# Kernel optimization log

Measured on AMD Instinct MI355X. Metric: run time of the kernel, lower is better.

Reference implementation:

```python
import jax, jax.numpy as jnp
import numpy as np

N_HITS = 49152
HIT_F = 256
INST_F = 32
N_IT_CONST = 1024
Q_MIN = 0.5   # ObjCondensationLoss default q_min
S_B = 1.0     # ObjCondensationLoss default background strength


def setup_inputs() -> dict:
    key = jax.random.key(0)
    ks = jax.random.split(key, 6)
    x = jax.random.normal(ks[0], (N_HITS, HIT_F), jnp.float32)
    W_beta = jax.random.normal(ks[1], (HIT_F, 1), jnp.float32) / np.sqrt(HIT_F).astype(np.float32)
    b_beta = jnp.zeros((1,), jnp.float32)
    W_coord = jax.random.normal(ks[2], (HIT_F, INST_F), jnp.float32) / np.sqrt(HIT_F).astype(np.float32)
    b_coord = jnp.zeros((INST_F,), jnp.float32)
    temp = jnp.zeros((), jnp.float32)  # nn.Parameter(torch.tensor(0.0))
    # true instance labels per hit; pin first N_IT hits so every instance is populated
    y_i = jax.random.randint(ks[3], (N_HITS,), 0, N_IT_CONST)
    y_i = y_i.at[:N_IT_CONST].set(jnp.arange(N_IT_CONST))
    idx = jnp.arange(N_HITS)
    noise = (idx % 5 == 0) & (idx >= N_IT_CONST)
    y_i = jnp.where(noise, -1, y_i).astype(jnp.int64)
    y_semantic = jax.random.randint(ks[4], (N_HITS,), 0, 7).astype(jnp.int32)
    # hit -> true-instance membership edges (E_H_IT), fixed shape built eagerly
    yv = np.asarray(y_i)
    e0 = np.nonzero(yv >= 0)[0]
    edge_index = jnp.asarray(np.stack([e0, yv[e0]]), dtype=jnp.int32)
    return {"x": x, "W_beta": W_beta, "b_beta": b_beta, "W_coord": W_coord,
            "b_coord": b_coord, "temp": temp, "y_i": y_i,
            "y_semantic": y_semantic, "edge_index": edge_index, "n_it": N_IT_CONST}


def _obj_condensation_loss(ox, beta, y_i, edge_index, n_it):
    """Object condensation loss -> stack([background_loss, potential_loss])."""
    n = ox.shape[0]
    beta_c = jnp.clip(beta, 1e-4, 1.0 - 1e-4)
    q = jnp.arctanh(beta_c) ** 2 + Q_MIN  # charge per hit, [N]
    e_h, e_i = edge_index[0], edge_index[1]
    qe = q[e_h]
    # condensation point alpha_k = member hit with max charge (segment argmax)
    seg_max = jax.ops.segment_max(qe, e_i, num_segments=n_it)
    is_max = qe >= seg_max[e_i]
    alpha = jax.ops.segment_min(jnp.where(is_max, e_h, n), e_i, num_segments=n_it)
    alpha = jnp.clip(alpha, 0, n - 1)
    x_a = ox[alpha]        # [K, D]
    q_a = q[alpha]         # [K]
    beta_a = beta_c[alpha]  # [K]
    # attractive potential over membership edges: q_i * q_alpha * ||x_i - x_alpha||^2
    d2_att = jnp.sum((ox[e_h] - x_a[e_i]) ** 2, axis=-1)
    v_att = jnp.sum(qe * q_a[e_i] * d2_att)
    # repulsive potential over all (hit, instance) non-member pairs: hinge(1 - dist)
    d2 = (jnp.sum(ox * ox, axis=1)[:, None] + jnp.sum(x_a * x_a, axis=1)[None, :]
          - 2.0 * ox @ x_a.T)  # [N, K]
    dist = jnp.sqrt(jnp.maximum(d2, 0.0) + 1e-12)
    hinge = jnp.maximum(1.0 - dist, 0.0)
    member = jnp.zeros((n, n_it), jnp.float32).at[e_h, e_i].set(1.0)
    v_rep = jnp.sum((q[:, None] * q_a[None, :]) * hinge * (1.0 - member))
    l_v = (v_att + v_rep) / n
    # background loss: push beta_alpha -> 1, noise-hit beta -> 0
    noise = y_i < 0
    n_noise = jnp.maximum(jnp.sum(noise), 1)
    l_b = jnp.mean(1.0 - beta_a) + S_B * jnp.sum(jnp.where(noise, beta_c, 0.0)) / n_noise
    return jnp.stack([l_b, l_v])


def reference(x, W_beta, b_beta, W_coord, b_coord, temp, y_i, y_semantic, edge_index, n_it):
    beta = jax.nn.sigmoid(x @ W_beta + b_beta)[:, 0]  # h.of, [N]
    ox = x @ W_coord + b_coord                        # h.ox, [N, D]
    loss_vec = _obj_condensation_loss(ox, beta, y_i, edge_index, n_it)
    loss_vec = loss_vec * jnp.exp(-temp)  # temperature-weighted (b, v)
    return loss_vec.sum() + temp          # train-stage scalar loss
```

## Files before the change

kernel.cpp:

```cpp
#include <hip/hip_runtime.h>
#include <math.h>

#define NH 49152
#define KI 1024
#define DD 32
#define HF 256

#define WS_PART   0
#define WS_SEGMAX 8
#define WS_ALPHA  (WS_SEGMAX + KI)
#define WS_XA     (WS_ALPHA + KI)
#define WS_A12    (WS_XA + KI*DD)
#define WS_H12    (WS_A12 + KI*12)
#define WS_OX     (WS_H12 + NH*12)

__global__ void k_init(float* __restrict__ ws) {
    int i = blockIdx.x * blockDim.x + threadIdx.x;
    if (i < KI) {
        ws[WS_SEGMAX + i] = 0.0f;
        ((int*)ws)[WS_ALPHA + i] = NH;
    }
    if (i < 8) ws[WS_PART + i] = 0.0f;
}

__global__ __launch_bounds__(256, 2) void k_gemm(
        const float* __restrict__ x, const float* __restrict__ Wb,
        const float* __restrict__ bb, const float* __restrict__ Wc,
        const float* __restrict__ bcrd, const int* __restrict__ yi,
        float* __restrict__ ws) {
    __shared__ float wl[256 * 36];
    __shared__ float xs[64 * 65];
    const int t  = threadIdx.x;
    const int hl = t & 63;
    const int g  = t >> 6;
    const int h0 = blockIdx.x * 64;

    #pragma unroll
    for (int c4 = 0; c4 < 8; ++c4)
        *(float4*)(wl + t * 36 + c4 * 4) = *(const float4*)(Wc + t * 32 + c4 * 4);
    wl[t * 36 + 32] = Wb[t];

    const int srow = t >> 4;
    const int scol = (t & 15) * 4;
    float4 r0, r1, r2, r3;
#define LOADC(kc) { \
        const float* xp = x + (size_t)(h0 + srow) * HF + (kc) * 64 + scol; \
        r0 = *(const float4*)(xp); \
        r1 = *(const float4*)(xp + 16 * HF); \
        r2 = *(const float4*)(xp + 32 * HF); \
        r3 = *(const float4*)(xp + 48 * HF); }
#define STOREC() { \
        float* d0p = xs + srow * 65 + scol; \
        d0p[0]=r0.x; d0p[1]=r0.y; d0p[2]=r0.z; d0p[3]=r0.w; \
        float* d1p = xs + (srow+16) * 65 + scol; \
        d1p[0]=r1.x; d1p[1]=r1.y; d1p[2]=r1.z; d1p[3]=r1.w; \
        float* d2p = xs + (srow+32) * 65 + scol; \
        d2p[0]=r2.x; d2p[1]=r2.y; d2p[2]=r2.z; d2p[3]=r2.w; \
        float* d3p = xs + (srow+48) * 65 + scol; \
        d3p[0]=r3.x; d3p[1]=r3.y; d3p[2]=r3.z; d3p[3]=r3.w; }

    float acc0 = 0.f, acc1 = 0.f, acc2 = 0.f, acc3 = 0.f;
    float acc4 = 0.f, acc5 = 0.f, acc6 = 0.f, acc7 = 0.f, acc8 = 0.f;

    LOADC(0);
    __syncthreads();
    STOREC();
    __syncthreads();

    for (int kc = 0; kc < 4; ++kc) {
        if (kc < 3) LOADC(kc + 1);
        const float* wbase = wl + kc * 64 * 36 + g * 8;
        #pragma unroll 8
        for (int kk = 0; kk < 64; ++kk) {
            float a = xs[hl * 65 + kk];
            const float4 w0 = *(const float4*)(wbase + kk * 36);
            const float4 w1 = *(const float4*)(wbase + kk * 36 + 4);
            acc0 = fmaf(a, w0.x, acc0);
            acc1 = fmaf(a, w0.y, acc1);
            acc2 = fmaf(a, w0.z, acc2);
            acc3 = fmaf(a, w0.w, acc3);
            acc4 = fmaf(a, w1.x, acc4);
            acc5 = fmaf(a, w1.y, acc5);
            acc6 = fmaf(a, w1.z, acc6);
            acc7 = fmaf(a, w1.w, acc7);
            if (g == 3) acc8 = fmaf(a, wbase[kk * 36 + 8], acc8);
        }
        __syncthreads();
        if (kc < 3) { STOREC(); __syncthreads(); }
    }

    const int h = h0 + hl;
    float4 o0, o1;
    o0.x = acc0 + bcrd[g * 8 + 0];
    o0.y = acc1 + bcrd[g * 8 + 1];
    o0.z = acc2 + bcrd[g * 8 + 2];
    o0.w = acc3 + bcrd[g * 8 + 3];
    o1.x = acc4 + bcrd[g * 8 + 4];
    o1.y = acc5 + bcrd[g * 8 + 5];
    o1.z = acc6 + bcrd[g * 8 + 6];
    o1.w = acc7 + bcrd[g * 8 + 7];
    *(float4*)(ws + WS_OX + (size_t)h * DD + g * 8)     = o0;
    *(float4*)(ws + WS_OX + (size_t)h * DD + g * 8 + 4) = o1;

    if (g == 0) {
        float s8 = o0.x*o0.x + o0.y*o0.y + o0.z*o0.z + o0.w*o0.w
                 + o1.x*o1.x + o1.y*o1.y + o1.z*o1.z + o1.w*o1.w;
        *(float4*)(ws + WS_H12 + (size_t)h * 12)     = o0;
        *(float4*)(ws + WS_H12 + (size_t)h * 12 + 4) = o1;
        ws[WS_H12 + (size_t)h * 12 + 8] = 0.5f * s8;
    }
    if (g == 3) {
        float z    = acc8 + bb[0];
        float beta = 1.0f / (1.0f + expf(-z));
        float bcv  = fminf(fmaxf(beta, 1e-4f), 0.9999f);
        float at   = atanhf(bcv);
        ws[WS_H12 + (size_t)h * 12 + 9]  = at * at + 0.5f;
        ws[WS_H12 + (size_t)h * 12 + 10] = bcv;
        int y = yi[h];
        float    nb  = (y < 0) ? bcv : 0.0f;
        unsigned cnt = (y < 0) ? 1u : 0u;
        for (int off = 32; off > 0; off >>= 1) {
            nb  += __shfl_down(nb, off);
            cnt += __shfl_down(cnt, off);
        }
        if (hl == 0) {
            atomicAdd(ws + WS_PART + 2, nb);
            atomicAdd((unsigned int*)(ws + WS_PART + 3), cnt);
        }
    }
}

__global__ __launch_bounds__(256) void k_segmax(const int* __restrict__ eh, const int* __restrict__ ei,
                                                int E, float* __restrict__ ws) {
    int e = blockIdx.x * 256 + threadIdx.x;
    if (e < E) {
        float qe = ws[WS_H12 + (size_t)eh[e] * 12 + 9];
        atomicMax((unsigned int*)(ws + WS_SEGMAX + ei[e]), __float_as_uint(qe));
    }
}

__global__ __launch_bounds__(256) void k_argmin(const int* __restrict__ eh, const int* __restrict__ ei,
                                                int E, float* __restrict__ ws) {
    int e = blockIdx.x * 256 + threadIdx.x;
    if (e < E) {
        float qe = ws[WS_H12 + (size_t)eh[e] * 12 + 9];
        if (qe >= ws[WS_SEGMAX + ei[e]])
            atomicMin((int*)ws + WS_ALPHA + ei[e], eh[e]);
    }
}

__global__ __launch_bounds__(1024) void k_gather(float* __restrict__ ws) {
    const int k = threadIdx.x;
    int a = ((int*)ws)[WS_ALPHA + k];
    a = min(a, NH - 1);
    float4 v0, v1;
    float s8 = 0.0f;
    #pragma unroll
    for (int d0 = 0; d0 < DD; d0 += 4) {
        float4 v = *(const float4*)(ws + WS_OX + (size_t)a * DD + d0);
        *(float4*)(ws + WS_XA + (size_t)k * DD + d0) = v;
        if (d0 == 0) { v0 = v; s8 += v.x*v.x + v.y*v.y + v.z*v.z + v.w*v.w; }
        if (d0 == 4) { v1 = v; s8 += v.x*v.x + v.y*v.y + v.z*v.z + v.w*v.w; }
    }
    *(float4*)(ws + WS_A12 + (size_t)k * 12)     = v0;
    *(float4*)(ws + WS_A12 + (size_t)k * 12 + 4) = v1;
    ws[WS_A12 + (size_t)k * 12 + 8] = 0.5f * (s8 - 1.0f);
    ws[WS_A12 + (size_t)k * 12 + 9] = ws[WS_H12 + (size_t)a * 12 + 9];
    float omba = 1.0f - ws[WS_H12 + (size_t)a * 12 + 10];
    for (int off = 32; off > 0; off >>= 1) omba += __shfl_down(omba, off);
    __shared__ float red[16];
    if ((k & 63) == 0) red[k >> 6] = omba;
    __syncthreads();
    if (k == 0) {
        float s = 0.0f;
        for (int i = 0; i < 16; ++i) s += red[i];
        atomicAdd(ws + WS_PART + 4, s);
    }
}

__global__ __launch_bounds__(256) void k_att(const int* __restrict__ eh, const int* __restrict__ ei,
                                             int E, float* __restrict__ ws) {
    const int t = threadIdx.x;
    const int e = blockIdx.x * 256 + t;
    float c = 0.0f;
    if (e < E) {
        const int h = eh[e], k = ei[e];
        const float* a = ws + WS_OX + (size_t)h * DD;
        const float* b = ws + WS_XA + (size_t)k * DD;
        float d2 = 0.0f;
        #pragma unroll
        for (int d0 = 0; d0 < DD; d0 += 4) {
            float4 av = *(const float4*)(a + d0);
            float4 bv = *(const float4*)(b + d0);
            float dx = av.x - bv.x; d2 = fmaf(dx, dx, d2);
            float dy = av.y - bv.y; d2 = fmaf(dy, dy, d2);
            float dz = av.z - bv.z; d2 = fmaf(dz, dz, d2);
            float dw = av.w - bv.w; d2 = fmaf(dw, dw, d2);
        }
        c = ws[WS_H12 + (size_t)h * 12 + 9] * ws[WS_A12 + (size_t)k * 12 + 9] * d2;
    }
    for (int off = 32; off > 0; off >>= 1) c += __shfl_down(c, off);
    __shared__ float red[4];
    if ((t & 63) == 0) red[t >> 6] = c;
    __syncthreads();
    if (t == 0) atomicAdd(ws + WS_PART + 1, red[0] + red[1] + red[2] + red[3]);
}

__global__ __launch_bounds__(256, 4) void k_rep(const int* __restrict__ yi, float* __restrict__ ws) {
    __shared__ float al[64 * 12];
    const int t  = threadIdx.x;
    const int bh = blockIdx.x % 96;
    const int bk = blockIdx.x / 96;

    for (int i = t; i < 64 * 12; i += 256)
        al[i] = ws[WS_A12 + (size_t)bk * 64 * 12 + i];
    __syncthreads();

    const int h1 = bh * 512 + t;
    const int h2 = h1 + 256;
    const float4 p0  = *(const float4*)(ws + WS_H12 + (size_t)h1 * 12);
    const float4 p1  = *(const float4*)(ws + WS_H12 + (size_t)h1 * 12 + 4);
    const float2 cq1 = *(const float2*)(ws + WS_H12 + (size_t)h1 * 12 + 8);
    const float4 s0  = *(const float4*)(ws + WS_H12 + (size_t)h2 * 12);
    const float4 s1  = *(const float4*)(ws + WS_H12 + (size_t)h2 * 12 + 4);
    const float2 cq2 = *(const float2*)(ws + WS_H12 + (size_t)h2 * 12 + 8);
    const int yh1 = yi[h1], yh2 = yi[h2];
    float loc = 0.0f;

    #pragma unroll 4
    for (int r = 0; r < 64; ++r) {
        const float4 b0  = *(const float4*)(al + r * 12);
        const float4 b1  = *(const float4*)(al + r * 12 + 4);
        const float2 bcq = *(const float2*)(al + r * 12 + 8);
        float acc1 = -cq1.x - bcq.x;
        acc1 = fmaf(p0.x, b0.x, acc1);
        acc1 = fmaf(p0.y, b0.y, acc1);
        acc1 = fmaf(p0.z, b0.z, acc1);
        acc1 = fmaf(p0.w, b0.w, acc1);
        acc1 = fmaf(p1.x, b1.x, acc1);
        acc1 = fmaf(p1.y, b1.y, acc1);
        acc1 = fmaf(p1.z, b1.z, acc1);
        acc1 = fmaf(p1.w, b1.w, acc1);
        float acc2 = -cq2.x - bcq.x;
        acc2 = fmaf(s0.x, b0.x, acc2);
        acc2 = fmaf(s0.y, b0.y, acc2);
        acc2 = fmaf(s0.z, b0.z, acc2);
        acc2 = fmaf(s0.w, b0.w, acc2);
        acc2 = fmaf(s1.x, b1.x, acc2);
        acc2 = fmaf(s1.y, b1.y, acc2);
        acc2 = fmaf(s1.z, b1.z, acc2);
        acc2 = fmaf(s1.w, b1.w, acc2);
        if (acc1 > 0.0f) {
            const int kg = bk * 64 + r;
            if (yh1 != kg) {
                float d2 = 1.0f - 2.0f * acc1;
                const float* hp = ws + WS_OX + (size_t)h1 * DD;
                const float* ap = ws + WS_XA + (size_t)kg * DD;
                #pragma unroll
                for (int d = 8; d < DD; d += 4) {
                    float4 av = *(const float4*)(hp + d);
                    float4 bv = *(const float4*)(ap + d);
                    float dx = av.x - bv.x; d2 = fmaf(dx, dx, d2);
                    float dy = av.y - bv.y; d2 = fmaf(dy, dy, d2);
                    float dz = av.z - bv.z; d2 = fmaf(dz, dz, d2);
                    float dw = av.w - bv.w; d2 = fmaf(dw, dw, d2);
                }
                float dist = sqrtf(fmaxf(d2, 0.0f) + 1e-12f);
                float hin  = 1.0f - dist;
                if (hin > 0.0f) loc += cq1.y * bcq.y * hin;
            }
        }
        if (acc2 > 0.0f) {
            const int kg = bk * 64 + r;
            if (yh2 != kg) {
                float d2 = 1.0f - 2.0f * acc2;
                const float* hp = ws + WS_OX + (size_t)h2 * DD;
                const float* ap = ws + WS_XA + (size_t)kg * DD;
                #pragma unroll
                for (int d = 8; d < DD; d += 4) {
                    float4 av = *(const float4*)(hp + d);
                    float4 bv = *(const float4*)(ap + d);
                    float dx = av.x - bv.x; d2 = fmaf(dx, dx, d2);
                    float dy = av.y - bv.y; d2 = fmaf(dy, dy, d2);
                    float dz = av.z - bv.z; d2 = fmaf(dz, dz, d2);
                    float dw = av.w - bv.w; d2 = fmaf(dw, dw, d2);
                }
                float dist = sqrtf(fmaxf(d2, 0.0f) + 1e-12f);
                float hin  = 1.0f - dist;
                if (hin > 0.0f) loc += cq2.y * bcq.y * hin;
            }
        }
    }
    for (int off = 32; off > 0; off >>= 1) loc += __shfl_down(loc, off);
    __shared__ float red[4];
    if ((t & 63) == 0) red[t >> 6] = loc;
    __syncthreads();
    if (t == 0) atomicAdd(ws + WS_PART + 0, red[0] + red[1] + red[2] + red[3]);
}

__global__ void k_final(const float* __restrict__ temp, float* __restrict__ ws,
                        float* __restrict__ out) {
    float vrep  = ws[WS_PART + 0];
    float vatt  = ws[WS_PART + 1];
    float nsum  = ws[WS_PART + 2];
    unsigned nn = *(const unsigned int*)(ws + WS_PART + 3);
    float somba = ws[WS_PART + 4];
    float lb = somba * (1.0f / (float)KI) + nsum / (float)(nn < 1u ? 1u : nn);
    float lv = (vatt + vrep) / (float)NH;
    float tv = temp[0];
    out[0] = (lb + lv) * expf(-tv) + tv;
}

extern "C" void kernel_launch(void* const* d_in, const int* in_sizes, int n_in,
                              void* d_out, int out_size, void* d_ws, size_t ws_size,
                              hipStream_t stream) {
    const float* x    = (const float*)d_in[0];
    const float* Wb   = (const float*)d_in[1];
    const float* bb   = (const float*)d_in[2];
    const float* Wc   = (const float*)d_in[3];
    const float* bcrd = (const float*)d_in[4];
    const float* temp = (const float*)d_in[5];
    const int*   yi   = (const int*)d_in[6];
    const int*   ep   = (const int*)d_in[8];
    const int E = in_sizes[8] / 2;
    const int* eh = ep;
    const int* ei = ep + E;
    float* ws  = (float*)d_ws;
    float* out = (float*)d_out;

    k_init<<<(KI + 255) / 256, 256, 0, stream>>>(ws);
    k_gemm<<<NH / 64, 256, 0, stream>>>(x, Wb, bb, Wc, bcrd, yi, ws);
    const int eb = (E + 255) / 256;
    k_segmax<<<eb, 256, 0, stream>>>(eh, ei, E, ws);
    k_argmin<<<eb, 256, 0, stream>>>(eh, ei, E, ws);
    k_gather<<<1, 1024, 0, stream>>>(ws);
    k_att<<<eb, 256, 0, stream>>>(eh, ei, E, ws);
    k_rep<<<96 * 16, 256, 0, stream>>>(yi, ws);
    k_final<<<1, 1, 0, stream>>>(temp, ws, out);
}
```

Before: 117.7 us.

## Retile projection GEMM, fuse segment argmax via packed 64-bit atomic, restructure repulsion

Several changes land at once. The projection GEMM now computes two hits per thread over 128-hit blocks, using a swizzled transposed shared tile with double buffering and reading weights directly from global memory. The segment max and argmin passes are merged into one 64-bit atomicMax on packed (charge, inverted index), which drops a kernel launch and a second pass over the edges. The gather runs across multiple blocks, and the repulsion kernel reads instance data straight from global memory over 128 instances per block with fewer blocks. The costs are more register pressure, uncached weight reads that rely on L1/L2, and a changed workspace layout.

```diff
diff --git a/kernel.cpp b/kernel.cpp
--- a/kernel.cpp
+++ b/kernel.cpp
@@ -6,21 +6,40 @@
 #define DD 32
 #define HF 256
 
-#define WS_PART   0
-#define WS_SEGMAX 8
-#define WS_ALPHA  (WS_SEGMAX + KI)
-#define WS_XA     (WS_ALPHA + KI)
-#define WS_A12    (WS_XA + KI*DD)
-#define WS_H12    (WS_A12 + KI*12)
-#define WS_OX     (WS_H12 + NH*12)
+#define WS_PART  0
+#define WS_SEG64 8
+#define WS_A12   (WS_SEG64 + 2*KI)
+#define WS_H12   (WS_A12 + 12*KI)
+#define WS_XA    (WS_H12 + 12*NH)
+#define WS_OX    (WS_XA + KI*DD)
 
 __global__ void k_init(float* __restrict__ ws) {
     int i = blockIdx.x * blockDim.x + threadIdx.x;
-    if (i < KI) {
-        ws[WS_SEGMAX + i] = 0.0f;
-        ((int*)ws)[WS_ALPHA + i] = NH;
-    }
+    if (i < KI) ((unsigned long long*)(ws + WS_SEG64))[i] = 0ull;
     if (i < 8) ws[WS_PART + i] = 0.0f;
+}
+
+template<bool G3>
+__device__ __forceinline__ void chunk_compute(const float (*xs)[128], int l, int kbase, int g,
+        const float* __restrict__ Wc, const float* __restrict__ Wb,
+        float* acc, float& wA, float& wB) {
+    #pragma unroll 8
+    for (int kk = 0; kk < 32; ++kk) {
+        const int K = ((kk >> 2) & 7) << 2;
+        const float2 xv = *(const float2*)(&xs[kk][(2 * l) ^ K]);
+        const int krow = kbase + kk;
+        const float4 w0 = *(const float4*)(Wc + krow * 32 + g * 8);
+        const float4 w1 = *(const float4*)(Wc + krow * 32 + g * 8 + 4);
+        acc[0] = fmaf(xv.x, w0.x, acc[0]);   acc[8]  = fmaf(xv.y, w0.x, acc[8]);
+        acc[1] = fmaf(xv.x, w0.y, acc[1]);   acc[9]  = fmaf(xv.y, w0.y, acc[9]);
+        acc[2] = fmaf(xv.x, w0.z, acc[2]);   acc[10] = fmaf(xv.y, w0.z, acc[10]);
+        acc[3] = fmaf(xv.x, w0.w, acc[3]);   acc[11] = fmaf(xv.y, w0.w, acc[11]);
+        acc[4] = fmaf(xv.x, w1.x, acc[4]);   acc[12] = fmaf(xv.y, w1.x, acc[12]);
+        acc[5] = fmaf(xv.x, w1.y, acc[5]);   acc[13] = fmaf(xv.y, w1.y, acc[13]);
+        acc[6] = fmaf(xv.x, w1.z, acc[6]);   acc[14] = fmaf(xv.y, w1.z, acc[14]);
+        acc[7] = fmaf(xv.x, w1.w, acc[7]);   acc[15] = fmaf(xv.y, w1.w, acc[15]);
+        if (G3) { const float wb = Wb[krow]; wA = fmaf(xv.x, wb, wA); wB = fmaf(xv.y, wb, wB); }
+    }
 }
 
 __global__ __launch_bounds__(256, 2) void k_gemm(
@@ -28,102 +47,89 @@
         const float* __restrict__ bb, const float* __restrict__ Wc,
         const float* __restrict__ bcrd, const int* __restrict__ yi,
         float* __restrict__ ws) {
-    __shared__ float wl[256 * 36];
-    __shared__ float xs[64 * 65];
+    __shared__ float xsT[2][32][128];
     const int t  = threadIdx.x;
-    const int hl = t & 63;
-    const int g  = t >> 6;
-    const int h0 = blockIdx.x * 64;
-
+    const int g  = __builtin_amdgcn_readfirstlane(t >> 6);
+    const int l  = t & 63;
+    const int h0 = blockIdx.x * 128;
+
+    const int sh = t >> 3;
+    const int sq = t & 7;
+    const int c0 = sh ^ (sq << 2);
+    float4 r0, r1, r2, r3;
+#define GLOAD(kc) { \
+    const float* xp = x + (size_t)(h0 + sh) * HF + (kc) * 32 + sq * 4; \
+    r0 = *(const float4*)(xp); \
+    r1 = *(const float4*)(xp + 32 * HF); \
+    r2 = *(const float4*)(xp + 64 * HF); \
+    r3 = *(const float4*)(xp + 96 * HF); }
+#define SSTORE(buf) { \
+    float* bp = &xsT[buf][sq * 4][0]; \
+    bp[c0]          = r0.x; bp[128 + c0]        = r0.y; bp[256 + c0]        = r0.z; bp[384 + c0]        = r0.w; \
+    bp[c0 + 32]     = r1.x; bp[128 + c0 + 32]   = r1.y; bp[256 + c0 + 32]   = r1.z; bp[384 + c0 + 32]   = r1.w; \
+    bp[c0 + 64]     = r2.x; bp[128 + c0 + 64]   = r2.y; bp[256 + c0 + 64]   = r2.z; bp[384 + c0 + 64]   = r2.w; \
+    bp[c0 + 96]     = r3.x; bp[128 + c0 + 96]   = r3.y; bp[256 + c0 + 96]   = r3.z; bp[384 + c0 + 96]   = r3.w; }
+
+    float acc[16];
     #pragma unroll
-    for (int c4 = 0; c4 < 8; ++c4)
-        *(float4*)(wl + t * 36 + c4 * 4) = *(const float4*)(Wc + t * 32 + c4 * 4);
-    wl[t * 36 + 32] = Wb[t];
-
-    const int srow = t >> 4;
-    const int scol = (t & 15) * 4;
-    float4 r0, r1, r2, r3;
-#define LOADC(kc) { \
-        const float* xp = x + (size_t)(h0 + srow) * HF + (kc) * 64 + scol; \
-        r0 = *(const float4*)(xp); \
-        r1 = *(const float4*)(xp + 16 * HF); \
-        r2 = *(const float4*)(xp + 32 * HF); \
-        r3 = *(const float4*)(xp + 48 * HF); }
-#define STOREC() { \
-        float* d0p = xs + srow * 65 + scol; \
-        d0p[0]=r0.x; d0p[1]=r0.y; d0p[2]=r0.z; d0p[3]=r0.w; \
-        float* d1p = xs + (srow+16) * 65 + scol; \
-        d1p[0]=r1.x; d1p[1]=r1.y; d1p[2]=r1.z; d1p[3]=r1.w; \
-        float* d2p = xs + (srow+32) * 65 + scol; \
-        d2p[0]=r2.x; d2p[1]=r2.y; d2p[2]=r2.z; d2p[3]=r2.w; \
-        float* d3p = xs + (srow+48) * 65 + scol; \
-        d3p[0]=r3.x; d3p[1]=r3.y; d3p[2]=r3.z; d3p[3]=r3.w; }
-
-    float acc0 = 0.f, acc1 = 0.f, acc2 = 0.f, acc3 = 0.f;
-    float acc4 = 0.f, acc5 = 0.f, acc6 = 0.f, acc7 = 0.f, acc8 = 0.f;
-
-    LOADC(0);
+    for (int i = 0; i < 16; ++i) acc[i] = 0.0f;
+    float wA = 0.0f, wB = 0.0f;
+
+    GLOAD(0);
+    SSTORE(0);
     __syncthreads();
-    STOREC();
-    __syncthreads();
-
-    for (int kc = 0; kc < 4; ++kc) {
-        if (kc < 3) LOADC(kc + 1);
-        const float* wbase = wl + kc * 64 * 36 + g * 8;
-        #pragma unroll 8
-        for (int kk = 0; kk < 64; ++kk) {
-            float a = xs[hl * 65 + kk];
-            const float4 w0 = *(const float4*)(wbase + kk * 36);
-            const float4 w1 = *(const float4*)(wbase + kk * 36 + 4);
-            acc0 = fmaf(a, w0.x, acc0);
-            acc1 = fmaf(a, w0.y, acc1);
-            acc2 = fmaf(a, w0.z, acc2);
-            acc3 = fmaf(a, w0.w, acc3);
-            acc4 = fmaf(a, w1.x, acc4);
-            acc5 = fmaf(a, w1.y, acc5);
-            acc6 = fmaf(a, w1.z, acc6);
-            acc7 = fmaf(a, w1.w, acc7);
-            if (g == 3) acc8 = fmaf(a, wbase[kk * 36 + 8], acc8);
-        }
+    for (int kc = 0; kc < 8; ++kc) {
+        if (kc < 7) GLOAD(kc + 1);
+        if (g == 3) chunk_compute<true>(xsT[kc & 1], l, kc * 32, g, Wc, Wb, acc, wA, wB);
+        else        chunk_compute<false>(xsT[kc & 1], l, kc * 32, g, Wc, Wb, acc, wA, wB);
         __syncthreads();
-        if (kc < 3) { STOREC(); __syncthreads(); }
-    }
-
-    const int h = h0 + hl;
-    float4 o0, o1;
-    o0.x = acc0 + bcrd[g * 8 + 0];
-    o0.y = acc1 + bcrd[g * 8 + 1];
-    o0.z = acc2 + bcrd[g * 8 + 2];
-    o0.w = acc3 + bcrd[g * 8 + 3];
-    o1.x = acc4 + bcrd[g * 8 + 4];
-    o1.y = acc5 + bcrd[g * 8 + 5];
-    o1.z = acc6 + bcrd[g * 8 + 6];
-    o1.w = acc7 + bcrd[g * 8 + 7];
-    *(float4*)(ws + WS_OX + (size_t)h * DD + g * 8)     = o0;
-    *(float4*)(ws + WS_OX + (size_t)h * DD + g * 8 + 4) = o1;
+        if (kc < 7) { SSTORE((kc + 1) & 1); __syncthreads(); }
+    }
+
+    const int ha = h0 + 2 * l;
+    const float4 bc0 = *(const float4*)(bcrd + g * 8);
+    const float4 bc1 = *(const float4*)(bcrd + g * 8 + 4);
+    float4 A0 = {acc[0] + bc0.x, acc[1] + bc0.y, acc[2] + bc0.z, acc[3] + bc0.w};
+    float4 A1 = {acc[4] + bc1.x, acc[5] + bc1.y, acc[6] + bc1.z, acc[7] + bc1.w};
+    float4 B0 = {acc[8] + bc0.x, acc[9] + bc0.y, acc[10] + bc0.z, acc[11] + bc0.w};
+    float4 B1 = {acc[12] + bc1.x, acc[13] + bc1.y, acc[14] + bc1.z, acc[15] + bc1.w};
+    *(float4*)(ws + WS_OX + (size_t)ha * DD + g * 8)           = A0;
+    *(float4*)(ws + WS_OX + (size_t)ha * DD + g * 8 + 4)       = A1;
+    *(float4*)(ws + WS_OX + (size_t)(ha + 1) * DD + g * 8)     = B0;
+    *(float4*)(ws + WS_OX + (size_t)(ha + 1) * DD + g * 8 + 4) = B1;
 
     if (g == 0) {
-        float s8 = o0.x*o0.x + o0.y*o0.y + o0.z*o0.z + o0.w*o0.w
-                 + o1.x*o1.x + o1.y*o1.y + o1.z*o1.z + o1.w*o1.w;
-        *(float4*)(ws + WS_H12 + (size_t)h * 12)     = o0;
-        *(float4*)(ws + WS_H12 + (size_t)h * 12 + 4) = o1;
-        ws[WS_H12 + (size_t)h * 12 + 8] = 0.5f * s8;
+        float sA = A0.x*A0.x + A0.y*A0.y + A0.z*A0.z + A0.w*A0.w
+                 + A1.x*A1.x + A1.y*A1.y + A1.z*A1.z + A1.w*A1.w;
+        float sB = B0.x*B0.x + B0.y*B0.y + B0.z*B0.z + B0.w*B0.w
+                 + B1.x*B1.x + B1.y*B1.y + B1.z*B1.z + B1.w*B1.w;
+        *(float4*)(ws + WS_H12 + (size_t)ha * 12)           = A0;
+        *(float4*)(ws + WS_H12 + (size_t)ha * 12 + 4)       = A1;
+        ws[WS_H12 + (size_t)ha * 12 + 8] = 0.5f * sA;
+        *(float4*)(ws + WS_H12 + (size_t)(ha + 1) * 12)     = B0;
+        *(float4*)(ws + WS_H12 + (size_t)(ha + 1) * 12 + 4) = B1;
+        ws[WS_H12 + (size_t)(ha + 1) * 12 + 8] = 0.5f * sB;
     }
     if (g == 3) {
-        float z    = acc8 + bb[0];
-        float beta = 1.0f / (1.0f + expf(-z));
-        float bcv  = fminf(fmaxf(beta, 1e-4f), 0.9999f);
-        float at   = atanhf(bcv);
-        ws[WS_H12 + (size_t)h * 12 + 9]  = at * at + 0.5f;
-        ws[WS_H12 + (size_t)h * 12 + 10] = bcv;
-        int y = yi[h];
-        float    nb  = (y < 0) ? bcv : 0.0f;
-        unsigned cnt = (y < 0) ? 1u : 0u;
+        const float bb0 = bb[0];
+        float zA = wA + bb0, zB = wB + bb0;
+        float bA = 1.0f / (1.0f + expf(-zA));
+        float bB = 1.0f / (1.0f + expf(-zB));
+        float bcA = fminf(fmaxf(bA, 1e-4f), 0.9999f);
+        float bcB = fminf(fmaxf(bB, 1e-4f), 0.9999f);
+        float atA = atanhf(bcA), atB = atanhf(bcB);
+        ws[WS_H12 + (size_t)ha * 12 + 9]        = atA * atA + 0.5f;
+        ws[WS_H12 + (size_t)ha * 12 + 10]       = bcA;
+        ws[WS_H12 + (size_t)(ha + 1) * 12 + 9]  = atB * atB + 0.5f;
+        ws[WS_H12 + (size_t)(ha + 1) * 12 + 10] = bcB;
+        int yA = yi[ha], yB = yi[ha + 1];
+        float    nb  = ((yA < 0) ? bcA : 0.0f) + ((yB < 0) ? bcB : 0.0f);
+        unsigned cnt = (unsigned)(yA < 0) + (unsigned)(yB < 0);
         for (int off = 32; off > 0; off >>= 1) {
             nb  += __shfl_down(nb, off);
             cnt += __shfl_down(cnt, off);
         }
-        if (hl == 0) {
+        if (l == 0) {
             atomicAdd(ws + WS_PART + 2, nb);
             atomicAdd((unsigned int*)(ws + WS_PART + 3), cnt);
         }
@@ -131,28 +137,23 @@
 }
 
 __global__ __launch_bounds__(256) void k_segmax(const int* __restrict__ eh, const int* __restrict__ ei,
-                                                int E, float* __restrict__ ws) {
+                                                int E, const float* __restrict__ h12,
+                                                unsigned long long* __restrict__ seg) {
     int e = blockIdx.x * 256 + threadIdx.x;
     if (e < E) {
-        float qe = ws[WS_H12 + (size_t)eh[e] * 12 + 9];
-        atomicMax((unsigned int*)(ws + WS_SEGMAX + ei[e]), __float_as_uint(qe));
-    }
-}
-
-__global__ __launch_bounds__(256) void k_argmin(const int* __restrict__ eh, const int* __restrict__ ei,
-                                                int E, float* __restrict__ ws) {
-    int e = blockIdx.x * 256 + threadIdx.x;
-    if (e < E) {
-        float qe = ws[WS_H12 + (size_t)eh[e] * 12 + 9];
-        if (qe >= ws[WS_SEGMAX + ei[e]])
-            atomicMin((int*)ws + WS_ALPHA + ei[e], eh[e]);
-    }
-}
-
-__global__ __launch_bounds__(1024) void k_gather(float* __restrict__ ws) {
-    const int k = threadIdx.x;
-    int a = ((int*)ws)[WS_ALPHA + k];
-    a = min(a, NH - 1);
+        int h = eh[e];
+        float q = h12[(size_t)h * 12 + 9];
+        unsigned long long pk = ((unsigned long long)__float_as_uint(q) << 32)
+                              | (unsigned)(NH - 1 - h);
+        atomicMax(seg + ei[e], pk);
+    }
+}
+
+__global__ __launch_bounds__(256) void k_gather(float* __restrict__ ws) {
+    const int k = blockIdx.x * 256 + threadIdx.x;
+    unsigned long long pk = ((const unsigned long long*)(ws + WS_SEG64))[k];
+    int a = NH - 1 - (int)(unsigned)(pk & 0xffffffffu);
+    a = max(0, min(a, NH - 1));
     float4 v0, v1;
     float s8 = 0.0f;
     #pragma unroll
@@ -168,14 +169,7 @@
     ws[WS_A12 + (size_t)k * 12 + 9] = ws[WS_H12 + (size_t)a * 12 + 9];
     float omba = 1.0f - ws[WS_H12 + (size_t)a * 12 + 10];
     for (int off = 32; off > 0; off >>= 1) omba += __shfl_down(omba, off);
-    __shared__ float red[16];
-    if ((k & 63) == 0) red[k >> 6] = omba;
-    __syncthreads();
-    if (k == 0) {
-        float s = 0.0f;
-        for (int i = 0; i < 16; ++i) s += red[i];
-        atomicAdd(ws + WS_PART + 4, s);
-    }
+    if ((threadIdx.x & 63) == 0) atomicAdd(ws + WS_PART + 4, omba);
 }
 
 __global__ __launch_bounds__(256) void k_att(const int* __restrict__ eh, const int* __restrict__ ei,
@@ -206,32 +200,32 @@
     if (t == 0) atomicAdd(ws + WS_PART + 1, red[0] + red[1] + red[2] + red[3]);
 }
 
-__global__ __launch_bounds__(256, 4) void k_rep(const int* __restrict__ yi, float* __restrict__ ws) {
-    __shared__ float al[64 * 12];
+__global__ __launch_bounds__(256, 3) void k_rep(const int* __restrict__ yi,
+        const float* __restrict__ a12, const float* __restrict__ h12,
+        const float* __restrict__ ox, const float* __restrict__ xa,
+        float* __restrict__ part) {
     const int t  = threadIdx.x;
     const int bh = blockIdx.x % 96;
     const int bk = blockIdx.x / 96;
-
-    for (int i = t; i < 64 * 12; i += 256)
-        al[i] = ws[WS_A12 + (size_t)bk * 64 * 12 + i];
-    __syncthreads();
+    const int k0 = bk * 128;
 
     const int h1 = bh * 512 + t;
     const int h2 = h1 + 256;
-    const float4 p0  = *(const float4*)(ws + WS_H12 + (size_t)h1 * 12);
-    const float4 p1  = *(const float4*)(ws + WS_H12 + (size_t)h1 * 12 + 4);
-    const float2 cq1 = *(const float2*)(ws + WS_H12 + (size_t)h1 * 12 + 8);
-    const float4 s0  = *(const float4*)(ws + WS_H12 + (size_t)h2 * 12);
-    const float4 s1  = *(const float4*)(ws + WS_H12 + (size_t)h2 * 12 + 4);
-    const float2 cq2 = *(const float2*)(ws + WS_H12 + (size_t)h2 * 12 + 8);
+    const float4 p0  = *(const float4*)(h12 + (size_t)h1 * 12);
+    const float4 p1  = *(const float4*)(h12 + (size_t)h1 * 12 + 4);
+    const float2 cq1 = *(const float2*)(h12 + (size_t)h1 * 12 + 8);
+    const float4 s0  = *(const float4*)(h12 + (size_t)h2 * 12);
+    const float4 s1  = *(const float4*)(h12 + (size_t)h2 * 12 + 4);
+    const float2 cq2 = *(const float2*)(h12 + (size_t)h2 * 12 + 8);
     const int yh1 = yi[h1], yh2 = yi[h2];
     float loc = 0.0f;
 
     #pragma unroll 4
-    for (int r = 0; r < 64; ++r) {
-        const float4 b0  = *(const float4*)(al + r * 12);
-        const float4 b1  = *(const float4*)(al + r * 12 + 4);
-        const float2 bcq = *(const float2*)(al + r * 12 + 8);
+    for (int r = 0; r < 128; ++r) {
+        const float* ap = a12 + (size_t)(k0 + r) * 12;
+        const float4 b0  = *(const float4*)(ap);
+        const float4 b1  = *(const float4*)(ap + 4);
+        const float2 bcq = *(const float2*)(ap + 8);
         float acc1 = -cq1.x - bcq.x;
         acc1 = fmaf(p0.x, b0.x, acc1);
         acc1 = fmaf(p0.y, b0.y, acc1);
@@ -251,15 +245,15 @@
         acc2 = fmaf(s1.z, b1.z, acc2);
         acc2 = fmaf(s1.w, b1.w, acc2);
         if (acc1 > 0.0f) {
-            const int kg = bk * 64 + r;
+            const int kg = k0 + r;
             if (yh1 != kg) {
                 float d2 = 1.0f - 2.0f * acc1;
-                const float* hp = ws + WS_OX + (size_t)h1 * DD;
-                const float* ap = ws + WS_XA + (size_t)kg * DD;
+                const float* hp = ox + (size_t)h1 * DD;
+                const float* apf = xa + (size_t)kg * DD;
                 #pragma unroll
                 for (int d = 8; d < DD; d += 4) {
                     float4 av = *(const float4*)(hp + d);
-                    float4 bv = *(const float4*)(ap + d);
+                    float4 bv = *(const float4*)(apf + d);
                     float dx = av.x - bv.x; d2 = fmaf(dx, dx, d2);
                     float dy = av.y - bv.y; d2 = fmaf(dy, dy, d2);
                     float dz = av.z - bv.z; d2 = fmaf(dz, dz, d2);
@@ -271,15 +265,15 @@
             }
         }
         if (acc2 > 0.0f) {
-            const int kg = bk * 64 + r;
+            const int kg = k0 + r;
             if (yh2 != kg) {
                 float d2 = 1.0f - 2.0f * acc2;
-                const float* hp = ws + WS_OX + (size_t)h2 * DD;
-                const float* ap = ws + WS_XA + (size_t)kg * DD;
+                const float* hp = ox + (size_t)h2 * DD;
+                const float* apf = xa + (size_t)kg * DD;
                 #pragma unroll
                 for (int d = 8; d < DD; d += 4) {
                     float4 av = *(const float4*)(hp + d);
-                    float4 bv = *(const float4*)(ap + d);
+                    float4 bv = *(const float4*)(apf + d);
                     float dx = av.x - bv.x; d2 = fmaf(dx, dx, d2);
                     float dy = av.y - bv.y; d2 = fmaf(dy, dy, d2);
                     float dz = av.z - bv.z; d2 = fmaf(dz, dz, d2);
@@ -295,7 +289,7 @@
     __shared__ float red[4];
     if ((t & 63) == 0) red[t >> 6] = loc;
     __syncthreads();
-    if (t == 0) atomicAdd(ws + WS_PART + 0, red[0] + red[1] + red[2] + red[3]);
+    if (t == 0) atomicAdd(part + 0, red[0] + red[1] + red[2] + red[3]);
 }
 
 __global__ void k_final(const float* __restrict__ temp, float* __restrict__ ws,
@@ -328,13 +322,14 @@
     float* ws  = (float*)d_ws;
     float* out = (float*)d_out;
 
-    k_init<<<(KI + 255) / 256, 256, 0, stream>>>(ws);
-    k_gemm<<<NH / 64, 256, 0, stream>>>(x, Wb, bb, Wc, bcrd, yi, ws);
+    k_init<<<4, 256, 0, stream>>>(ws);
+    k_gemm<<<NH / 128, 256, 0, stream>>>(x, Wb, bb, Wc, bcrd, yi, ws);
     const int eb = (E + 255) / 256;
-    k_segmax<<<eb, 256, 0, stream>>>(eh, ei, E, ws);
-    k_argmin<<<eb, 256, 0, stream>>>(eh, ei, E, ws);
-    k_gather<<<1, 1024, 0, stream>>>(ws);
+    k_segmax<<<eb, 256, 0, stream>>>(eh, ei, E, ws + WS_H12,
+                                     (unsigned long long*)(ws + WS_SEG64));
+    k_gather<<<KI / 256, 256, 0, stream>>>(ws);
     k_att<<<eb, 256, 0, stream>>>(eh, ei, E, ws);
-    k_rep<<<96 * 16, 256, 0, stream>>>(yi, ws);
+    k_rep<<<96 * 8, 256, 0, stream>>>(yi, ws + WS_A12, ws + WS_H12,
+                                      ws + WS_OX, ws + WS_XA, ws);
     k_final<<<1, 1, 0, stream>>>(temp, ws, out);
 }
```

Result: faster. 97.27 us (-17.3%).
